# Performance work log

Measured on AMD Instinct MI355X. Metric: run time of the kernel, lower is better.

## Reference

```python
import jax, jax.numpy as jnp
import numpy as np

N_ATOMS = 10000
N_PAIR = 100000
F = 128
N_HEAD = 4
FH = F // N_HEAD  # 32
DEGREES = [1, 2, 3]
N_DEG = len(DEGREES)
REPEATS = np.array([2 * l + 1 for l in DEGREES])  # [3,5,7]
M_TOT = int(REPEATS.sum())  # 15
K_RBF = 32


def ssp(x):
    # shifted softplus: softplus(x) - log(2)
    return jax.nn.softplus(x) - jnp.log(2.0).astype(x.dtype)


def setup_inputs() -> dict:
    key = jax.random.key(0)
    ks = jax.random.split(key, 16)
    inp = {
        "x": jax.random.normal(ks[0], (N_ATOMS, F), jnp.float32),
        "rbf_ij": jax.random.normal(ks[1], (N_PAIR, K_RBF), jnp.float32),
        "sph_ij": jax.random.normal(ks[2], (N_PAIR, M_TOT), jnp.float32),
        "phi_r_cut": jax.random.uniform(ks[3], (N_PAIR,), jnp.float32),
        "idx_i": jnp.sort(jax.random.randint(ks[4], (N_PAIR,), 0, N_ATOMS)),
        "idx_j": jax.random.randint(ks[5], (N_PAIR,), 0, N_ATOMS),
        "pair_mask": jnp.ones((N_PAIR,), jnp.float32),
        # params
        "W_Q": jax.random.normal(ks[6], (N_DEG, N_HEAD, FH, FH), jnp.float32) / np.sqrt(FH),
        "W_K": jax.random.normal(ks[7], (N_DEG, N_HEAD, FH, FH), jnp.float32) / np.sqrt(FH),
        # in2f MLP: single dense F -> F
        "W_in": jax.random.normal(ks[8], (F, F), jnp.float32) / np.sqrt(F),
        "b_in": jnp.zeros((F,), jnp.float32),
        # radial filter MLP: K -> K (ssp) -> n_deg*F
        "W_f1": jax.random.normal(ks[9], (K_RBF, K_RBF), jnp.float32) / np.sqrt(K_RBF),
        "b_f1": jnp.zeros((K_RBF,), jnp.float32),
        "W_f2": jax.random.normal(ks[10], (K_RBF, N_DEG * F), jnp.float32) / np.sqrt(K_RBF),
        "b_f2": jnp.zeros((N_DEG * F,), jnp.float32),
        # f2out MLP: single dense F -> F
        "W_out": jax.random.normal(ks[11], (F, F), jnp.float32) / np.sqrt(F),
        "b_out": jnp.zeros((F,), jnp.float32),
    }
    return inp


def reference(x, rbf_ij, sph_ij, phi_r_cut, idx_i, idx_j, pair_mask,
              W_Q, W_K, W_in, b_in, W_f1, b_f1, W_f2, b_f2, W_out, b_out):
    n = x.shape[0]
    # in2f embedding (last in2f dim == F)
    x_f = x @ W_in + b_in                                  # (n, F)
    x_head = x_f.reshape(n, N_HEAD, FH)                    # (n, h, FH)

    # per-degree, per-head linear maps (the nested vmap matmuls)
    Q = jnp.einsum('dhij,nhj->ndhi', W_Q, x_head)          # (n, n_deg, h, FH)
    K = jnp.einsum('dhij,nhj->ndhi', W_K, x_head)

    m = pair_mask[:, None, None, None]
    Q_i = Q[idx_i] * m                                     # (P, n_deg, h, FH)
    K_j = K[idx_j] * m

    # radial filter: MLP(rbf) -> (P, n_deg, h, FH), scaled by cutoff
    h1 = ssp(rbf_ij @ W_f1 + b_f1)
    W_ij = (h1 @ W_f2 + b_f2).reshape(-1, N_DEG, N_HEAD, FH)
    W_ij = W_ij * phi_r_cut[:, None, None, None]

    # attention coefficients per degree/head
    alpha = jnp.sum(Q_i * K_j * W_ij, axis=-1)             # (P, n_deg, h)
    alpha = jnp.repeat(alpha, repeats=REPEATS, axis=1, total_repeat_length=M_TOT)  # (P, m_tot, h)
    alpha = alpha / jnp.sqrt(jnp.asarray(FH, x.dtype))     # att_scale

    # outer product of neighbor features with spherical harmonics
    x_j = x_head[idx_j] * pair_mask[:, None, None]         # (P, h, FH)
    z_ij = jnp.einsum('pm,phf->pmhf', sph_ij, x_j)         # (P, m_tot, h, FH)
    z_ij = alpha[:, :, :, None] * z_ij
    z_ij = z_ij.reshape(z_ij.shape[0], M_TOT, F)           # (P, m_tot, F)

    agg = jax.ops.segment_sum(z_ij, idx_i, num_segments=n)  # (n, m_tot, F)

    # f2out projection (last f2out dim == F)
    out = agg @ W_out + b_out                               # (n, m_tot, F)
    return out
```

## Files before the change

kernel.cpp:

```cpp
#include <hip/hip_runtime.h>
#include <hip/hip_bf16.h>

#define N_ATOMS 10000
#define N_PAIR  100000
#define F_DIM   128
#define N_HEAD  4
#define FH      32
#define N_DEG   3
#define M_TOT   15
#define K_RBF   32
#define R_OUT   (N_ATOMS * M_TOT)

typedef __attribute__((ext_vector_type(8))) short short8;
typedef __attribute__((ext_vector_type(4))) float f32x4;

union frag_cast { int i[4]; short8 s; };

__device__ __forceinline__ float sspf(float v) {
    float sp = fmaxf(v, 0.f) + log1pf(expf(-fabsf(v)));
    return sp - 0.69314718055994531f;
}

__device__ __forceinline__ unsigned short bf16_rne(float x) {
    unsigned int u = __float_as_uint(x);
    unsigned int r = u + 0x7fffu + ((u >> 16) & 1u);
    return (unsigned short)(r >> 16);
}
__device__ __forceinline__ float bf16_tof(unsigned short h) {
    return __uint_as_float(((unsigned int)h) << 16);
}

__global__ __launch_bounds__(256) void k_gemm128(
    const float* __restrict__ A, const float* __restrict__ B,
    const float* __restrict__ bias, float* __restrict__ C, int rows)
{
    __shared__ float As[32][132];
    __shared__ float Bs[32][132];
    int r0 = blockIdx.x * 128;
    int t = threadIdx.x;
    int ty = t >> 4, tx = t & 15;

    float acc[8][8];
    #pragma unroll
    for (int i = 0; i < 8; ++i)
        #pragma unroll
        for (int j = 0; j < 8; ++j) acc[i][j] = 0.f;

    for (int k0 = 0; k0 < 128; k0 += 32) {
        #pragma unroll
        for (int r = 0; r < 16; ++r) {
            int idx = t + 256 * r;
            int row = idx >> 5, kk = idx & 31;
            int grow = r0 + row;
            As[kk][row] = (grow < rows) ? A[grow * 128 + k0 + kk] : 0.f;
        }
        #pragma unroll
        for (int r = 0; r < 16; ++r) {
            int idx = t + 256 * r;
            int kk = idx >> 7, c = idx & 127;
            Bs[kk][c] = B[(k0 + kk) * 128 + c];
        }
        __syncthreads();

        #pragma unroll
        for (int kk = 0; kk < 32; ++kk) {
            float a[8], b[8];
            *(float4*)&a[0] = *(const float4*)&As[kk][ty * 4];
            *(float4*)&a[4] = *(const float4*)&As[kk][64 + ty * 4];
            *(float4*)&b[0] = *(const float4*)&Bs[kk][tx * 4];
            *(float4*)&b[4] = *(const float4*)&Bs[kk][64 + tx * 4];
            #pragma unroll
            for (int i = 0; i < 8; ++i)
                #pragma unroll
                for (int j = 0; j < 8; ++j)
                    acc[i][j] = fmaf(a[i], b[j], acc[i][j]);
        }
        __syncthreads();
    }

    float bj[8];
    #pragma unroll
    for (int j = 0; j < 4; ++j) { bj[j] = bias[tx * 4 + j]; bj[4 + j] = bias[64 + tx * 4 + j]; }

    #pragma unroll
    for (int i = 0; i < 8; ++i) {
        int row = r0 + ((i < 4) ? (ty * 4 + i) : (64 + ty * 4 + (i - 4)));
        if (row < rows) {
            float4 v0, v1;
            v0.x = acc[i][0] + bj[0]; v0.y = acc[i][1] + bj[1];
            v0.z = acc[i][2] + bj[2]; v0.w = acc[i][3] + bj[3];
            v1.x = acc[i][4] + bj[4]; v1.y = acc[i][5] + bj[5];
            v1.z = acc[i][6] + bj[6]; v1.w = acc[i][7] + bj[7];
            *(float4*)&C[row * 128 + tx * 4] = v0;
            *(float4*)&C[row * 128 + 64 + tx * 4] = v1;
        }
    }
}

__global__ __launch_bounds__(384) void k_qk(
    const float* __restrict__ xh, const float* __restrict__ W_Q,
    const float* __restrict__ W_K, float* __restrict__ Q, float* __restrict__ K)
{
    __shared__ float xfs[32][128];
    int t = threadIdx.x;
    int h = (t >> 5) & 3;
    float wq[32], wk[32];
    const float4* wqp = (const float4*)(W_Q + t * 32);
    const float4* wkp = (const float4*)(W_K + t * 32);
    #pragma unroll
    for (int j4 = 0; j4 < 8; ++j4) {
        float4 a = wqp[j4], b = wkp[j4];
        wq[4 * j4 + 0] = a.x; wq[4 * j4 + 1] = a.y; wq[4 * j4 + 2] = a.z; wq[4 * j4 + 3] = a.w;
        wk[4 * j4 + 0] = b.x; wk[4 * j4 + 1] = b.y; wk[4 * j4 + 2] = b.z; wk[4 * j4 + 3] = b.w;
    }
    int ab = blockIdx.x * 32;
    for (int idx = t; idx < 4096; idx += 384) {
        int aa = idx >> 7, f = idx & 127;
        int ag = ab + aa;
        xfs[aa][f] = (ag < N_ATOMS) ? xh[ag * 128 + f] : 0.f;
    }
    __syncthreads();
    for (int aa = 0; aa < 32; ++aa) {
        int ag = ab + aa;
        if (ag >= N_ATOMS) break;
        const float4* xv = (const float4*)&xfs[aa][h * 32];
        float q0 = 0.f, q1 = 0.f, k0 = 0.f, k1 = 0.f;
        #pragma unroll
        for (int j4 = 0; j4 < 8; j4 += 2) {
            float4 x0 = xv[j4], x1 = xv[j4 + 1];
            q0 = fmaf(wq[4 * j4 + 0], x0.x, q0); q0 = fmaf(wq[4 * j4 + 1], x0.y, q0);
            q0 = fmaf(wq[4 * j4 + 2], x0.z, q0); q0 = fmaf(wq[4 * j4 + 3], x0.w, q0);
            q1 = fmaf(wq[4 * j4 + 4], x1.x, q1); q1 = fmaf(wq[4 * j4 + 5], x1.y, q1);
            q1 = fmaf(wq[4 * j4 + 6], x1.z, q1); q1 = fmaf(wq[4 * j4 + 7], x1.w, q1);
            k0 = fmaf(wk[4 * j4 + 0], x0.x, k0); k0 = fmaf(wk[4 * j4 + 1], x0.y, k0);
            k0 = fmaf(wk[4 * j4 + 2], x0.z, k0); k0 = fmaf(wk[4 * j4 + 3], x0.w, k0);
            k1 = fmaf(wk[4 * j4 + 4], x1.x, k1); k1 = fmaf(wk[4 * j4 + 5], x1.y, k1);
            k1 = fmaf(wk[4 * j4 + 6], x1.z, k1); k1 = fmaf(wk[4 * j4 + 7], x1.w, k1);
        }
        Q[ag * 384 + t] = q0 + q1;
        K[ag * 384 + t] = k0 + k1;
    }
}

__global__ __launch_bounds__(256) void k_cvt_w2(
    const float* __restrict__ W, unsigned short* __restrict__ Wh,
    unsigned short* __restrict__ Wl)
{
    int idx = blockIdx.x * 256 + threadIdx.x;
    if (idx < 12288) {
        int e = idx >> 5, k = idx & 31;
        float v = W[k * 384 + e];
        unsigned short h = bf16_rne(v);
        unsigned short l = bf16_rne(v - bf16_tof(h));
        Wh[e * 32 + k] = h;
        Wl[e * 32 + k] = l;
    }
}

__global__ __launch_bounds__(256) void k_pair(
    const float* __restrict__ rbf, const float* __restrict__ phi,
    const float* __restrict__ mask, const int* __restrict__ idx_i,
    const int* __restrict__ idx_j, const float* __restrict__ W_f1,
    const float* __restrict__ b_f1, const unsigned short* __restrict__ W2h,
    const unsigned short* __restrict__ W2l, const float* __restrict__ b_f2,
    const float* __restrict__ Q, const float* __restrict__ K,
    float* __restrict__ alpha)
{
    __shared__ float g_s[32][384];
    __shared__ unsigned int h1p_s[32][36];
    __shared__ int   i_s[32];
    __shared__ int   j_s[32];
    __shared__ float phim_s[32];

    float (*rbf_s)[33] = (float (*)[33])(&g_s[0][0]);
    float (*wf1_s)[33] = (float (*)[33])(&g_s[0][0] + 32 * 33);

    int t = threadIdx.x;
    int p0 = blockIdx.x * 32;

    for (int idx = t; idx < 1024; idx += 256) {
        int r = idx >> 5, c = idx & 31;
        rbf_s[r][c] = rbf[p0 * 32 + idx];
        wf1_s[r][c] = W_f1[idx];
    }
    if (t < 32) {
        int pg = p0 + t;
        i_s[t] = idx_i[pg];
        j_s[t] = idx_j[pg];
        float m = mask[pg];
        phim_s[t] = phi[pg] * m * m * 0.17677669529663687f;
    }
    __syncthreads();

    {
        int p = t >> 3, c4 = (t & 7) * 4;
        float acc0 = b_f1[c4 + 0], acc1 = b_f1[c4 + 1];
        float acc2 = b_f1[c4 + 2], acc3 = b_f1[c4 + 3];
        #pragma unroll
        for (int k = 0; k < 32; ++k) {
            float rv = rbf_s[p][k];
            acc0 = fmaf(rv, wf1_s[k][c4 + 0], acc0);
            acc1 = fmaf(rv, wf1_s[k][c4 + 1], acc1);
            acc2 = fmaf(rv, wf1_s[k][c4 + 2], acc2);
            acc3 = fmaf(rv, wf1_s[k][c4 + 3], acc3);
        }
        float hv[4] = {sspf(acc0), sspf(acc1), sspf(acc2), sspf(acc3)};
        #pragma unroll
        for (int j = 0; j < 4; ++j) {
            unsigned short hh = bf16_rne(hv[j]);
            unsigned short ll = bf16_rne(hv[j] - bf16_tof(hh));
            h1p_s[p][c4 + j] = ((unsigned int)hh << 16) | (unsigned int)ll;
        }
    }
    __syncthreads();

    #pragma unroll
    for (int it = 0; it < 12; ++it) {
        int idx = it * 256 + t;
        int p = idx / 96;
        int c4 = idx - p * 96;
        const float4* qp = (const float4*)(Q + i_s[p] * 384) + c4;
        const float4* kp = (const float4*)(K + j_s[p] * 384) + c4;
        float4 qv = *qp, kv = *kp;
        float4 gv;
        gv.x = qv.x * kv.x; gv.y = qv.y * kv.y;
        gv.z = qv.z * kv.z; gv.w = qv.w * kv.w;
        *(float4*)&g_s[p][c4 * 4] = gv;
    }
    __syncthreads();

    int wave = t >> 6, lane = t & 63;
    int quad = lane >> 4, l15 = lane & 15;

    short8 ah[2], al[2];
    #pragma unroll
    for (int mt = 0; mt < 2; ++mt) {
        const unsigned int* hp = &h1p_s[mt * 16 + l15][quad * 8];
        uint4 u01 = *(const uint4*)hp;
        uint4 u23 = *(const uint4*)(hp + 4);
        unsigned int u[8] = {u01.x, u01.y, u01.z, u01.w, u23.x, u23.y, u23.z, u23.w};
        frag_cast fh, fl;
        #pragma unroll
        for (int q = 0; q < 4; ++q) {
            unsigned int a0 = u[2 * q], a1 = u[2 * q + 1];
            fh.i[q] = (int)((a0 >> 16) | (a1 & 0xffff0000u));
            fl.i[q] = (int)((a0 & 0xffffu) | (a1 << 16));
        }
        ah[mt] = fh.s;
        al[mt] = fl.s;
    }

    #pragma unroll
    for (int dd = 0; dd < 3; ++dd) {
        int dh = wave * 3 + dd;
        int e_base = dh * 32;
        short8 bh0 = *(const short8*)(W2h + (e_base + l15) * 32 + quad * 8);
        short8 bl0 = *(const short8*)(W2l + (e_base + l15) * 32 + quad * 8);
        short8 bh1 = *(const short8*)(W2h + (e_base + 16 + l15) * 32 + quad * 8);
        short8 bl1 = *(const short8*)(W2l + (e_base + 16 + l15) * 32 + quad * 8);
        float b2v0 = b_f2[e_base + l15];
        float b2v1 = b_f2[e_base + 16 + l15];

        #pragma unroll
        for (int mt = 0; mt < 2; ++mt) {
            f32x4 s0 = {0.f, 0.f, 0.f, 0.f};
            f32x4 s1 = {0.f, 0.f, 0.f, 0.f};
            s0 = __builtin_amdgcn_mfma_f32_16x16x32_bf16(ah[mt], bh0, s0, 0, 0, 0);
            s1 = __builtin_amdgcn_mfma_f32_16x16x32_bf16(ah[mt], bh1, s1, 0, 0, 0);
            s0 = __builtin_amdgcn_mfma_f32_16x16x32_bf16(al[mt], bh0, s0, 0, 0, 0);
            s1 = __builtin_amdgcn_mfma_f32_16x16x32_bf16(al[mt], bh1, s1, 0, 0, 0);
            s0 = __builtin_amdgcn_mfma_f32_16x16x32_bf16(ah[mt], bl0, s0, 0, 0, 0);
            s1 = __builtin_amdgcn_mfma_f32_16x16x32_bf16(ah[mt], bl1, s1, 0, 0, 0);

            float vsum[4];
            #pragma unroll
            for (int r = 0; r < 4; ++r) {
                int prow = mt * 16 + quad * 4 + r;
                float v = (s0[r] + b2v0) * g_s[prow][e_base + l15]
                        + (s1[r] + b2v1) * g_s[prow][e_base + 16 + l15];
                #pragma unroll
                for (int off = 8; off >= 1; off >>= 1)
                    v += __shfl_xor(v, off, 16);
                vsum[r] = v;
            }
            if (l15 == 0) {
                #pragma unroll
                for (int r = 0; r < 4; ++r) {
                    int prow = mt * 16 + quad * 4 + r;
                    alpha[(p0 + prow) * 12 + dh] = vsum[r] * phim_s[prow];
                }
            }
        }
    }
}

__device__ __forceinline__ int lower_bound_i(const int* __restrict__ arr, int n, int val) {
    int lo = 0, hi = n;
    while (lo < hi) {
        int mid = (lo + hi) >> 1;
        if (arr[mid] < val) lo = mid + 1; else hi = mid;
    }
    return lo;
}

__global__ __launch_bounds__(256) void k_seg(const int* __restrict__ idx_i,
                                             int* __restrict__ seg)
{
    int a = blockIdx.x * 256 + threadIdx.x;
    if (a <= N_ATOMS) seg[a] = lower_bound_i(idx_i, N_PAIR, a);
}

__global__ __launch_bounds__(256) void k_cvt_b(
    const float* __restrict__ W, unsigned short* __restrict__ Bth,
    unsigned short* __restrict__ Btl)
{
    int idx = blockIdx.x * 256 + threadIdx.x;
    int cc = idx >> 7, kk = idx & 127;
    float v = W[kk * 128 + cc];
    unsigned short h = bf16_rne(v);
    unsigned short l = bf16_rne(v - bf16_tof(h));
    Bth[cc * 128 + kk] = h;
    Btl[cc * 128 + kk] = l;
}

__global__ __launch_bounds__(256) void k_agg(
    const float* __restrict__ xh, const float* __restrict__ alpha,
    const float* __restrict__ sph, const int* __restrict__ seg,
    const int* __restrict__ idx_j, const float* __restrict__ mask,
    unsigned int* __restrict__ aggp)
{
    __shared__ float red[15][132];
    int a = blockIdx.x;
    int t = threadIdx.x & 127;
    int grp = threadIdx.x >> 7;
    int h = t >> 5;
    int lo = seg[a], hi = seg[a + 1];

    float acc[15];
    #pragma unroll
    for (int m = 0; m < 15; ++m) acc[m] = 0.f;

    int p = lo + grp;
    float x_cur = 0.f;
    if (p < hi) x_cur = xh[idx_j[p] * 128 + t];
    for (; p < hi; p += 2) {
        int pn = p + 2;
        float x_nxt = 0.f;
        if (pn < hi) x_nxt = xh[idx_j[pn] * 128 + t];
        float xj = x_cur * mask[p];
        float a0v = alpha[p * 12 + h];
        float a1v = alpha[p * 12 + 4 + h];
        float a2v = alpha[p * 12 + 8 + h];
        const float* sp = sph + p * 15;
        #pragma unroll
        for (int m = 0; m < 15; ++m) {
            float al = (m < 3) ? a0v : ((m < 8) ? a1v : a2v);
            acc[m] = fmaf(sp[m] * al, xj, acc[m]);
        }
        x_cur = x_nxt;
    }

    if (grp == 1) {
        #pragma unroll
        for (int m = 0; m < 15; ++m) red[m][t] = acc[m];
    }
    __syncthreads();
    if (grp == 0) {
        #pragma unroll
        for (int m = 0; m < 15; ++m) {
            float v = acc[m] + red[m][t];
            unsigned short hh = bf16_rne(v);
            unsigned short ll = bf16_rne(v - bf16_tof(hh));
            aggp[(a * 15 + m) * 128 + t] = ((unsigned int)hh << 16) | (unsigned int)ll;
        }
    }
}

__global__ __launch_bounds__(256) void k_out_mfma(
    const unsigned int* __restrict__ Apack,
    const unsigned short* __restrict__ Bth, const unsigned short* __restrict__ Btl,
    const float* __restrict__ bias, float* __restrict__ C)
{
    int t = threadIdx.x;
    int wave = t >> 6, lane = t & 63;
    int quad = lane >> 4, l15 = lane & 15;
    long rowbase = (long)blockIdx.x * 128 + wave * 32;

    short8 ah[2][4], al[2][4];
    #pragma unroll
    for (int rt = 0; rt < 2; ++rt) {
        long row = rowbase + rt * 16 + l15;
        if (row > R_OUT - 1) row = R_OUT - 1;
        #pragma unroll
        for (int ks = 0; ks < 4; ++ks) {
            const uint4* ap = (const uint4*)(Apack + row * 128 + ks * 32 + quad * 8);
            uint4 u01 = ap[0], u23 = ap[1];
            unsigned int u[8] = {u01.x, u01.y, u01.z, u01.w, u23.x, u23.y, u23.z, u23.w};
            frag_cast fh, fl;
            #pragma unroll
            for (int q = 0; q < 4; ++q) {
                unsigned int a0 = u[2 * q], a1 = u[2 * q + 1];
                fh.i[q] = (int)((a0 >> 16) | (a1 & 0xffff0000u));
                fl.i[q] = (int)((a0 & 0xffffu) | (a1 << 16));
            }
            ah[rt][ks] = fh.s;
            al[rt][ks] = fl.s;
        }
    }

    #pragma unroll 2
    for (int nt = 0; nt < 8; ++nt) {
        int colbase = nt * 16;
        short8 bh[4], bl[4];
        #pragma unroll
        for (int ks = 0; ks < 4; ++ks) {
            int off = (colbase + l15) * 128 + ks * 32 + quad * 8;
            bh[ks] = *(const short8*)(Bth + off);
            bl[ks] = *(const short8*)(Btl + off);
        }
        f32x4 acc0 = {0.f, 0.f, 0.f, 0.f};
        f32x4 acc1 = {0.f, 0.f, 0.f, 0.f};
        #pragma unroll
        for (int ks = 0; ks < 4; ++ks) {
            acc0 = __builtin_amdgcn_mfma_f32_16x16x32_bf16(ah[0][ks], bh[ks], acc0, 0, 0, 0);
            acc1 = __builtin_amdgcn_mfma_f32_16x16x32_bf16(ah[1][ks], bh[ks], acc1, 0, 0, 0);
            acc0 = __builtin_amdgcn_mfma_f32_16x16x32_bf16(al[0][ks], bh[ks], acc0, 0, 0, 0);
            acc1 = __builtin_amdgcn_mfma_f32_16x16x32_bf16(al[1][ks], bh[ks], acc1, 0, 0, 0);
            acc0 = __builtin_amdgcn_mfma_f32_16x16x32_bf16(ah[0][ks], bl[ks], acc0, 0, 0, 0);
            acc1 = __builtin_amdgcn_mfma_f32_16x16x32_bf16(ah[1][ks], bl[ks], acc1, 0, 0, 0);
        }
        float bv = bias[colbase + l15];
        #pragma unroll
        for (int r = 0; r < 4; ++r) {
            long row0 = rowbase + quad * 4 + r;
            long row1 = rowbase + 16 + quad * 4 + r;
            if (row0 < R_OUT) C[row0 * 128 + colbase + l15] = acc0[r] + bv;
            if (row1 < R_OUT) C[row1 * 128 + colbase + l15] = acc1[r] + bv;
        }
    }
}

extern "C" void kernel_launch(void* const* d_in, const int* in_sizes, int n_in,
                              void* d_out, int out_size, void* d_ws, size_t ws_size,
                              hipStream_t stream) {
    const float* x        = (const float*)d_in[0];
    const float* rbf_ij   = (const float*)d_in[1];
    const float* sph_ij   = (const float*)d_in[2];
    const float* phi_r    = (const float*)d_in[3];
    const int*   idx_i    = (const int*)d_in[4];
    const int*   idx_j    = (const int*)d_in[5];
    const float* pmask    = (const float*)d_in[6];
    const float* W_Q      = (const float*)d_in[7];
    const float* W_K      = (const float*)d_in[8];
    const float* W_in     = (const float*)d_in[9];
    const float* b_in     = (const float*)d_in[10];
    const float* W_f1     = (const float*)d_in[11];
    const float* b_f1     = (const float*)d_in[12];
    const float* W_f2     = (const float*)d_in[13];
    const float* b_f2     = (const float*)d_in[14];
    const float* W_out    = (const float*)d_in[15];
    const float* b_out    = (const float*)d_in[16];
    float* out = (float*)d_out;

    float* ws    = (float*)d_ws;
    float* xh    = ws;
    float* Qbuf  = xh + N_ATOMS * F_DIM;
    float* Kbuf  = Qbuf + N_ATOMS * 384;
    float* alpha = Kbuf + N_ATOMS * 384;
    int*   seg   = (int*)(alpha + N_PAIR * 12);
    unsigned short* Bth = (unsigned short*)(seg + 10432);
    unsigned short* Btl = Bth + 16384;
    unsigned short* W2h = Btl + 16384;
    unsigned short* W2l = W2h + 12288;

    k_seg<<<(N_ATOMS + 256) / 256, 256, 0, stream>>>(idx_i, seg);
    k_cvt_b<<<64, 256, 0, stream>>>(W_out, Bth, Btl);
    k_cvt_w2<<<48, 256, 0, stream>>>(W_f2, W2h, W2l);
    k_gemm128<<<(N_ATOMS + 127) / 128, 256, 0, stream>>>(x, W_in, b_in, xh, N_ATOMS);
    k_qk<<<(N_ATOMS + 31) / 32, 384, 0, stream>>>(xh, W_Q, W_K, Qbuf, Kbuf);
    k_pair<<<N_PAIR / 32, 256, 0, stream>>>(rbf_ij, phi_r, pmask, idx_i, idx_j,
                                            W_f1, b_f1, W2h, W2l, b_f2,
                                            Qbuf, Kbuf, alpha);
    k_agg<<<N_ATOMS, 256, 0, stream>>>(xh, alpha, sph_ij, seg, idx_j, pmask,
                                       (unsigned int*)d_out);
    k_out_mfma<<<(R_OUT + 127) / 128, 256, 0, stream>>>((const unsigned int*)d_out,
                                                        Bth, Btl, b_out, out);
}
```

Baseline: 374.5 us.

## Fuse segment aggregation with output projection and halve pair tile size

```diff
diff --git a/kernel.cpp b/kernel.cpp
--- a/kernel.cpp
+++ b/kernel.cpp
@@ -9,7 +9,6 @@
 #define N_DEG   3
 #define M_TOT   15
 #define K_RBF   32
-#define R_OUT   (N_ATOMS * M_TOT)
 
 typedef __attribute__((ext_vector_type(8))) short short8;
 typedef __attribute__((ext_vector_type(4))) float f32x4;
@@ -166,24 +165,27 @@
     const float* __restrict__ Q, const float* __restrict__ K,
     float* __restrict__ alpha)
 {
-    __shared__ float g_s[32][384];
-    __shared__ unsigned int h1p_s[32][36];
-    __shared__ int   i_s[32];
-    __shared__ int   j_s[32];
-    __shared__ float phim_s[32];
+    __shared__ float g_s[16][388];
+    __shared__ unsigned int h1p_s[16][36];
+    __shared__ int   i_s[16];
+    __shared__ int   j_s[16];
+    __shared__ float phim_s[16];
 
     float (*rbf_s)[33] = (float (*)[33])(&g_s[0][0]);
-    float (*wf1_s)[33] = (float (*)[33])(&g_s[0][0] + 32 * 33);
+    float (*wf1_s)[33] = (float (*)[33])(&g_s[0][0] + 16 * 33);
 
     int t = threadIdx.x;
-    int p0 = blockIdx.x * 32;
-
-    for (int idx = t; idx < 1024; idx += 256) {
-        int r = idx >> 5, c = idx & 31;
-        rbf_s[r][c] = rbf[p0 * 32 + idx];
-        wf1_s[r][c] = W_f1[idx];
-    }
-    if (t < 32) {
+    int p0 = blockIdx.x * 16;
+
+    for (int idx = t; idx < 1536; idx += 256) {
+        if (idx < 512) {
+            rbf_s[idx >> 5][idx & 31] = rbf[p0 * 32 + idx];
+        } else {
+            int k = idx - 512;
+            wf1_s[k >> 5][k & 31] = W_f1[k];
+        }
+    }
+    if (t < 16) {
         int pg = p0 + t;
         i_s[t] = idx_i[pg];
         j_s[t] = idx_j[pg];
@@ -193,29 +195,26 @@
     __syncthreads();
 
     {
-        int p = t >> 3, c4 = (t & 7) * 4;
-        float acc0 = b_f1[c4 + 0], acc1 = b_f1[c4 + 1];
-        float acc2 = b_f1[c4 + 2], acc3 = b_f1[c4 + 3];
+        int p = t >> 4, c0 = (t & 15) * 2;
+        float acc0 = b_f1[c0], acc1 = b_f1[c0 + 1];
         #pragma unroll
         for (int k = 0; k < 32; ++k) {
             float rv = rbf_s[p][k];
-            acc0 = fmaf(rv, wf1_s[k][c4 + 0], acc0);
-            acc1 = fmaf(rv, wf1_s[k][c4 + 1], acc1);
-            acc2 = fmaf(rv, wf1_s[k][c4 + 2], acc2);
-            acc3 = fmaf(rv, wf1_s[k][c4 + 3], acc3);
-        }
-        float hv[4] = {sspf(acc0), sspf(acc1), sspf(acc2), sspf(acc3)};
-        #pragma unroll
-        for (int j = 0; j < 4; ++j) {
-            unsigned short hh = bf16_rne(hv[j]);
-            unsigned short ll = bf16_rne(hv[j] - bf16_tof(hh));
-            h1p_s[p][c4 + j] = ((unsigned int)hh << 16) | (unsigned int)ll;
-        }
-    }
-    __syncthreads();
-
-    #pragma unroll
-    for (int it = 0; it < 12; ++it) {
+            acc0 = fmaf(rv, wf1_s[k][c0], acc0);
+            acc1 = fmaf(rv, wf1_s[k][c0 + 1], acc1);
+        }
+        float h0 = sspf(acc0), h1v = sspf(acc1);
+        unsigned short hh0 = bf16_rne(h0);
+        unsigned short ll0 = bf16_rne(h0 - bf16_tof(hh0));
+        unsigned short hh1 = bf16_rne(h1v);
+        unsigned short ll1 = bf16_rne(h1v - bf16_tof(hh1));
+        h1p_s[p][c0]     = ((unsigned int)hh0 << 16) | (unsigned int)ll0;
+        h1p_s[p][c0 + 1] = ((unsigned int)hh1 << 16) | (unsigned int)ll1;
+    }
+    __syncthreads();
+
+    #pragma unroll
+    for (int it = 0; it < 6; ++it) {
         int idx = it * 256 + t;
         int p = idx / 96;
         int c4 = idx - p * 96;
@@ -232,10 +231,9 @@
     int wave = t >> 6, lane = t & 63;
     int quad = lane >> 4, l15 = lane & 15;
 
-    short8 ah[2], al[2];
-    #pragma unroll
-    for (int mt = 0; mt < 2; ++mt) {
-        const unsigned int* hp = &h1p_s[mt * 16 + l15][quad * 8];
+    short8 ah, al;
+    {
+        const unsigned int* hp = &h1p_s[l15][quad * 8];
         uint4 u01 = *(const uint4*)hp;
         uint4 u23 = *(const uint4*)(hp + 4);
         unsigned int u[8] = {u01.x, u01.y, u01.z, u01.w, u23.x, u23.y, u23.z, u23.w};
@@ -246,8 +244,8 @@
             fh.i[q] = (int)((a0 >> 16) | (a1 & 0xffff0000u));
             fl.i[q] = (int)((a0 & 0xffffu) | (a1 << 16));
         }
-        ah[mt] = fh.s;
-        al[mt] = fl.s;
+        ah = fh.s;
+        al = fl.s;
     }
 
     #pragma unroll
@@ -261,34 +259,31 @@
         float b2v0 = b_f2[e_base + l15];
         float b2v1 = b_f2[e_base + 16 + l15];
 
-        #pragma unroll
-        for (int mt = 0; mt < 2; ++mt) {
-            f32x4 s0 = {0.f, 0.f, 0.f, 0.f};
-            f32x4 s1 = {0.f, 0.f, 0.f, 0.f};
-            s0 = __builtin_amdgcn_mfma_f32_16x16x32_bf16(ah[mt], bh0, s0, 0, 0, 0);
-            s1 = __builtin_amdgcn_mfma_f32_16x16x32_bf16(ah[mt], bh1, s1, 0, 0, 0);
-            s0 = __builtin_amdgcn_mfma_f32_16x16x32_bf16(al[mt], bh0, s0, 0, 0, 0);
-            s1 = __builtin_amdgcn_mfma_f32_16x16x32_bf16(al[mt], bh1, s1, 0, 0, 0);
-            s0 = __builtin_amdgcn_mfma_f32_16x16x32_bf16(ah[mt], bl0, s0, 0, 0, 0);
-            s1 = __builtin_amdgcn_mfma_f32_16x16x32_bf16(ah[mt], bl1, s1, 0, 0, 0);
-
-            float vsum[4];
+        f32x4 s0 = {0.f, 0.f, 0.f, 0.f};
+        f32x4 s1 = {0.f, 0.f, 0.f, 0.f};
+        s0 = __builtin_amdgcn_mfma_f32_16x16x32_bf16(ah, bh0, s0, 0, 0, 0);
+        s1 = __builtin_amdgcn_mfma_f32_16x16x32_bf16(ah, bh1, s1, 0, 0, 0);
+        s0 = __builtin_amdgcn_mfma_f32_16x16x32_bf16(al, bh0, s0, 0, 0, 0);
+        s1 = __builtin_amdgcn_mfma_f32_16x16x32_bf16(al, bh1, s1, 0, 0, 0);
+        s0 = __builtin_amdgcn_mfma_f32_16x16x32_bf16(ah, bl0, s0, 0, 0, 0);
+        s1 = __builtin_amdgcn_mfma_f32_16x16x32_bf16(ah, bl1, s1, 0, 0, 0);
+
+        float vsum[4];
+        #pragma unroll
+        for (int r = 0; r < 4; ++r) {
+            int prow = quad * 4 + r;
+            float v = (s0[r] + b2v0) * g_s[prow][e_base + l15]
+                    + (s1[r] + b2v1) * g_s[prow][e_base + 16 + l15];
+            #pragma unroll
+            for (int off = 8; off >= 1; off >>= 1)
+                v += __shfl_xor(v, off, 16);
+            vsum[r] = v;
+        }
+        if (l15 == 0) {
             #pragma unroll
             for (int r = 0; r < 4; ++r) {
-                int prow = mt * 16 + quad * 4 + r;
-                float v = (s0[r] + b2v0) * g_s[prow][e_base + l15]
-                        + (s1[r] + b2v1) * g_s[prow][e_base + 16 + l15];
-                #pragma unroll
-                for (int off = 8; off >= 1; off >>= 1)
-                    v += __shfl_xor(v, off, 16);
-                vsum[r] = v;
-            }
-            if (l15 == 0) {
-                #pragma unroll
-                for (int r = 0; r < 4; ++r) {
-                    int prow = mt * 16 + quad * 4 + r;
-                    alpha[(p0 + prow) * 12 + dh] = vsum[r] * phim_s[prow];
-                }
+                int prow = quad * 4 + r;
+                alpha[(p0 + prow) * 12 + dh] = vsum[r] * phim_s[prow];
             }
         }
     }
@@ -323,16 +318,21 @@
     Btl[cc * 128 + kk] = l;
 }
 
-__global__ __launch_bounds__(256) void k_agg(
+__global__ __launch_bounds__(512) void k_agg_out(
     const float* __restrict__ xh, const float* __restrict__ alpha,
     const float* __restrict__ sph, const int* __restrict__ seg,
     const int* __restrict__ idx_j, const float* __restrict__ mask,
-    unsigned int* __restrict__ aggp)
-{
-    __shared__ float red[15][132];
-    int a = blockIdx.x;
-    int t = threadIdx.x & 127;
-    int grp = threadIdx.x >> 7;
+    const unsigned short* __restrict__ Bth, const unsigned short* __restrict__ Btl,
+    const float* __restrict__ bias, float* __restrict__ C)
+{
+    __shared__ float red_s[2][15][132];
+    __shared__ unsigned int ap_s[2][16][132];
+
+    int tid = threadIdx.x;
+    int sub = tid >> 8;
+    int t   = tid & 127;
+    int grp = (tid >> 7) & 1;
+    int a = blockIdx.x * 2 + sub;
     int h = t >> 5;
     int lo = seg[a], hi = seg[a + 1];
 
@@ -362,80 +362,68 @@
 
     if (grp == 1) {
         #pragma unroll
-        for (int m = 0; m < 15; ++m) red[m][t] = acc[m];
+        for (int m = 0; m < 15; ++m) red_s[sub][m][t] = acc[m];
     }
     __syncthreads();
     if (grp == 0) {
         #pragma unroll
         for (int m = 0; m < 15; ++m) {
-            float v = acc[m] + red[m][t];
+            float v = acc[m] + red_s[sub][m][t];
             unsigned short hh = bf16_rne(v);
             unsigned short ll = bf16_rne(v - bf16_tof(hh));
-            aggp[(a * 15 + m) * 128 + t] = ((unsigned int)hh << 16) | (unsigned int)ll;
-        }
-    }
-}
-
-__global__ __launch_bounds__(256) void k_out_mfma(
-    const unsigned int* __restrict__ Apack,
-    const unsigned short* __restrict__ Bth, const unsigned short* __restrict__ Btl,
-    const float* __restrict__ bias, float* __restrict__ C)
-{
-    int t = threadIdx.x;
-    int wave = t >> 6, lane = t & 63;
+            ap_s[sub][m][t] = ((unsigned int)hh << 16) | (unsigned int)ll;
+        }
+        ap_s[sub][15][t] = 0u;
+    }
+    __syncthreads();
+
+    int wave = tid >> 6, lane = tid & 63;
     int quad = lane >> 4, l15 = lane & 15;
-    long rowbase = (long)blockIdx.x * 128 + wave * 32;
-
-    short8 ah[2][4], al[2][4];
-    #pragma unroll
-    for (int rt = 0; rt < 2; ++rt) {
-        long row = rowbase + rt * 16 + l15;
-        if (row > R_OUT - 1) row = R_OUT - 1;
+    int am = wave >> 2;
+    int cb = (wave & 3) * 32;
+    long ga = (long)blockIdx.x * 2 + am;
+
+    short8 ah[4], al[4];
+    #pragma unroll
+    for (int ks = 0; ks < 4; ++ks) {
+        const unsigned int* hp = &ap_s[am][l15][ks * 32 + quad * 8];
+        uint4 u01 = *(const uint4*)hp;
+        uint4 u23 = *(const uint4*)(hp + 4);
+        unsigned int u[8] = {u01.x, u01.y, u01.z, u01.w, u23.x, u23.y, u23.z, u23.w};
+        frag_cast fh, fl;
+        #pragma unroll
+        for (int q = 0; q < 4; ++q) {
+            unsigned int a0 = u[2 * q], a1 = u[2 * q + 1];
+            fh.i[q] = (int)((a0 >> 16) | (a1 & 0xffff0000u));
+            fl.i[q] = (int)((a0 & 0xffffu) | (a1 << 16));
+        }
+        ah[ks] = fh.s;
+        al[ks] = fl.s;
+    }
+
+    #pragma unroll
+    for (int ct = 0; ct < 2; ++ct) {
+        int c = cb + ct * 16;
+        short8 bh[4], bl[4];
         #pragma unroll
         for (int ks = 0; ks < 4; ++ks) {
-            const uint4* ap = (const uint4*)(Apack + row * 128 + ks * 32 + quad * 8);
-            uint4 u01 = ap[0], u23 = ap[1];
-            unsigned int u[8] = {u01.x, u01.y, u01.z, u01.w, u23.x, u23.y, u23.z, u23.w};
-            frag_cast fh, fl;
-            #pragma unroll
-            for (int q = 0; q < 4; ++q) {
-                unsigned int a0 = u[2 * q], a1 = u[2 * q + 1];
-                fh.i[q] = (int)((a0 >> 16) | (a1 & 0xffff0000u));
-                fl.i[q] = (int)((a0 & 0xffffu) | (a1 << 16));
-            }
-            ah[rt][ks] = fh.s;
-            al[rt][ks] = fl.s;
-        }
-    }
-
-    #pragma unroll 2
-    for (int nt = 0; nt < 8; ++nt) {
-        int colbase = nt * 16;
-        short8 bh[4], bl[4];
-        #pragma unroll
-        for (int ks = 0; ks < 4; ++ks) {
-            int off = (colbase + l15) * 128 + ks * 32 + quad * 8;
+            int off = (c + l15) * 128 + ks * 32 + quad * 8;
             bh[ks] = *(const short8*)(Bth + off);
             bl[ks] = *(const short8*)(Btl + off);
         }
-        f32x4 acc0 = {0.f, 0.f, 0.f, 0.f};
-        f32x4 acc1 = {0.f, 0.f, 0.f, 0.f};
+        f32x4 oacc = {0.f, 0.f, 0.f, 0.f};
         #pragma unroll
         for (int ks = 0; ks < 4; ++ks) {
-            acc0 = __builtin_amdgcn_mfma_f32_16x16x32_bf16(ah[0][ks], bh[ks], acc0, 0, 0, 0);
-            acc1 = __builtin_amdgcn_mfma_f32_16x16x32_bf16(ah[1][ks], bh[ks], acc1, 0, 0, 0);
-            acc0 = __builtin_amdgcn_mfma_f32_16x16x32_bf16(al[0][ks], bh[ks], acc0, 0, 0, 0);
-            acc1 = __builtin_amdgcn_mfma_f32_16x16x32_bf16(al[1][ks], bh[ks], acc1, 0, 0, 0);
-            acc0 = __builtin_amdgcn_mfma_f32_16x16x32_bf16(ah[0][ks], bl[ks], acc0, 0, 0, 0);
-            acc1 = __builtin_amdgcn_mfma_f32_16x16x32_bf16(ah[1][ks], bl[ks], acc1, 0, 0, 0);
-        }
-        float bv = bias[colbase + l15];
+            oacc = __builtin_amdgcn_mfma_f32_16x16x32_bf16(ah[ks], bh[ks], oacc, 0, 0, 0);
+            oacc = __builtin_amdgcn_mfma_f32_16x16x32_bf16(al[ks], bh[ks], oacc, 0, 0, 0);
+            oacc = __builtin_amdgcn_mfma_f32_16x16x32_bf16(ah[ks], bl[ks], oacc, 0, 0, 0);
+        }
+        float bv = bias[c + l15];
         #pragma unroll
         for (int r = 0; r < 4; ++r) {
-            long row0 = rowbase + quad * 4 + r;
-            long row1 = rowbase + 16 + quad * 4 + r;
-            if (row0 < R_OUT) C[row0 * 128 + colbase + l15] = acc0[r] + bv;
-            if (row1 < R_OUT) C[row1 * 128 + colbase + l15] = acc1[r] + bv;
+            int row = quad * 4 + r;
+            if (row < 15)
+                C[(ga * 15 + row) * 128 + c + l15] = oacc[r] + bv;
         }
     }
 }
@@ -478,11 +466,9 @@
     k_cvt_w2<<<48, 256, 0, stream>>>(W_f2, W2h, W2l);
     k_gemm128<<<(N_ATOMS + 127) / 128, 256, 0, stream>>>(x, W_in, b_in, xh, N_ATOMS);
     k_qk<<<(N_ATOMS + 31) / 32, 384, 0, stream>>>(xh, W_Q, W_K, Qbuf, Kbuf);
-    k_pair<<<N_PAIR / 32, 256, 0, stream>>>(rbf_ij, phi_r, pmask, idx_i, idx_j,
+    k_pair<<<N_PAIR / 16, 256, 0, stream>>>(rbf_ij, phi_r, pmask, idx_i, idx_j,
                                             W_f1, b_f1, W2h, W2l, b_f2,
                                             Qbuf, Kbuf, alpha);
-    k_agg<<<N_ATOMS, 256, 0, stream>>>(xh, alpha, sph_ij, seg, idx_j, pmask,
-                                       (unsigned int*)d_out);
-    k_out_mfma<<<(R_OUT + 127) / 128, 256, 0, stream>>>((const unsigned int*)d_out,
-                                                        Bth, Btl, b_out, out);
-}
+    k_agg_out<<<N_ATOMS / 2, 512, 0, stream>>>(xh, alpha, sph_ij, seg, idx_j, pmask,
+                                               Bth, Btl, b_out, out);
+}
```

Result: slower. 391.5 us (+4.5%).
